# Optimization experiments

Hardware: AMD Instinct MI355X
Metric: run time of the kernel (lower is better)

## Reference

```python
import jax, jax.numpy as jnp
import numpy as np

B, N, I, H, NT = 512, 21, 256, 1024, 5  # batch, nodes, input, hidden, node types
EPS = 1e-12


def setup_inputs() -> dict:
    key = jax.random.key(0)
    ks = jax.random.split(key, 8)
    stdv = 1.0 / np.sqrt(H)
    return {
        "input": jax.random.normal(ks[0], (B, N, I), jnp.float32),
        "hx": 0.1 * jax.random.normal(ks[1], (B, N, H), jnp.float32),
        "cx": 0.1 * jax.random.normal(ks[2], (B, N, H), jnp.float32),
        "G": jnp.eye(N, dtype=jnp.float32) + 0.01 * jax.random.normal(ks[3], (N, N), jnp.float32),
        "weight_ih": jax.random.uniform(ks[4], (NT, 4 * H, I), jnp.float32, -stdv, stdv),
        "weight_hh": jax.random.uniform(ks[5], (NT, 4 * H, H), jnp.float32, -stdv, stdv),
        "bias_hh": jax.random.uniform(ks[6], (NT, 4 * H), jnp.float32, -stdv, stdv),
        "node_types": jax.random.randint(ks[7], (N,), 0, NT),
        "t": 3,
    }


def _l1_normalize_rows(g):
    # torch.nn.functional.normalize(g, p=1, dim=1)
    return g / jnp.maximum(jnp.sum(jnp.abs(g), axis=1, keepdims=True), EPS)


def _clockwork_phase(hidden_size, dtype):
    p = jnp.arange(hidden_size, dtype=dtype)
    p = p / p[-1] * 8.0 + 1.0
    return jnp.floor(p)  # values in {1..9}


def reference(input, hx, cx, G, weight_ih, weight_hh, bias_hh, node_types, t):
    # learn_influence=True -> gx = L1-row-normalized G
    gx = _l1_normalize_rows(G)

    # per-node-type weight gather: [N, 4H, I], [N, 4H, H], [N, 4H]
    w_ih = weight_ih[node_types]
    w_hh = weight_hh[node_types]
    b_hh = bias_hh[node_types]

    # gmm: einsum('ndo,bnd->bno', w.transpose(-2,-1), x) == einsum('noi,bni->bno', w, x)
    gates = (jnp.einsum('noi,bni->bno', w_ih, input)
             + jnp.einsum('noh,bnh->bno', w_hh, hx)
             + b_hh)
    # graph influence: matmul(gx, gates) over node dim -> [B, N, 4H]
    gates = jnp.einsum('mn,bno->bmo', gx, gates)

    ingate, forgetgate, cellgate, outgate = jnp.split(gates, 4, axis=2)
    ingate = jax.nn.sigmoid(ingate)
    forgetgate = jax.nn.sigmoid(forgetgate)
    cellgate = jnp.tanh(cellgate)
    outgate = jax.nn.sigmoid(outgate)

    phase = _clockwork_phase(hx.shape[-1], cx.dtype)
    c_mask = (jnp.remainder(jnp.float32(t) + 1.0, phase) < 0.01).astype(cx.dtype)

    cy = c_mask * (forgetgate * cx + ingate * cellgate) + (1.0 - c_mask) * cx
    hy = outgate * jnp.tanh(cy)

    # gx = gx + G_add (=0), then re-normalized because learn_influence=True
    gx_out = _l1_normalize_rows(gx)
    return hy, cy, gx_out
```

## Files before the change

kernel.cpp:

```cpp
#include <hip/hip_runtime.h>
#include <hip/hip_bf16.h>
#include <stdint.h>


typedef __bf16 bf16_t;
typedef __bf16 bf16x8 __attribute__((ext_vector_type(8)));
typedef float f32x4 __attribute__((ext_vector_type(4)));

#define NB 512
#define NN 21
#define NI 256
#define NH 1024
#define KDIM 1280
#define ODIM 4096
#define BNH (512ull * 21 * 1024)

__device__ inline void gld16(const void* g, const void* l) {
  __builtin_amdgcn_global_load_lds(
      (const __attribute__((address_space(1))) unsigned int*)g,
      (__attribute__((address_space(3))) unsigned int*)l, 16, 0, 0);
}

__device__ inline float sigmoid_fast(float x) {
  return 1.0f / (1.0f + __expf(-x));
}
__device__ inline float tanh_fast(float x) {
  float ax = fabsf(x);
  float e = __expf(2.0f * ax);
  float t = 1.0f - 2.0f / (e + 1.0f);
  return copysignf(t, x);
}

__global__ void gx_kernel(const float* __restrict__ G, float* __restrict__ gxw,
                          float* __restrict__ gxout) {
  int m = threadIdx.x;
  if (m < NN) {
    float s = 0.f;
    for (int j = 0; j < NN; j++) s += fabsf(G[m * NN + j]);
    s = fmaxf(s, 1e-12f);
    float row[NN];
    float s2 = 0.f;
    for (int j = 0; j < NN; j++) {
      row[j] = G[m * NN + j] / s;
      s2 += fabsf(row[j]);
    }
    s2 = fmaxf(s2, 1e-12f);
    for (int j = 0; j < NN; j++) {
      gxw[m * NN + j] = row[j];
      gxout[m * NN + j] = row[j] / s2;
    }
  }
}

__global__ __launch_bounds__(256) void pack_w(const float* __restrict__ wih,
                                              const float* __restrict__ whh,
                                              bf16_t* __restrict__ Wc) {
  int c = blockIdx.x * 256 + threadIdx.x;
  int k8 = c % (KDIM / 8);
  int row = c / (KDIM / 8);
  int k = k8 * 8;
  const float* src = (k < NI) ? (wih + (size_t)row * NI + k)
                              : (whh + (size_t)row * NH + (k - NI));
  float4 a = *(const float4*)src;
  float4 b = *(const float4*)(src + 4);
  bf16x8 o;
  o[0] = (bf16_t)a.x; o[1] = (bf16_t)a.y; o[2] = (bf16_t)a.z; o[3] = (bf16_t)a.w;
  o[4] = (bf16_t)b.x; o[5] = (bf16_t)b.y; o[6] = (bf16_t)b.z; o[7] = (bf16_t)b.w;
  *(bf16x8*)&Wc[(size_t)c * 8] = o;
}

__global__ __launch_bounds__(256) void pack_x(const float* __restrict__ input,
                                              const float* __restrict__ hx,
                                              bf16_t* __restrict__ Xc) {
  int c = blockIdx.x * 256 + threadIdx.x;
  int k8 = c % (KDIM / 8);
  int rest = c / (KDIM / 8);
  int n = rest / NB;
  int b = rest % NB;
  int k = k8 * 8;
  const float* src = (k < NI) ? (input + ((size_t)b * NN + n) * NI + k)
                              : (hx + ((size_t)b * NN + n) * NH + (k - NI));
  float4 a = *(const float4*)src;
  float4 d = *(const float4*)(src + 4);
  bf16x8 o;
  o[0] = (bf16_t)a.x; o[1] = (bf16_t)a.y; o[2] = (bf16_t)a.z; o[3] = (bf16_t)a.w;
  o[4] = (bf16_t)d.x; o[5] = (bf16_t)d.y; o[6] = (bf16_t)d.z; o[7] = (bf16_t)d.w;
  *(bf16x8*)&Xc[(size_t)c * 8] = o;
}

__global__ __launch_bounds__(256) void gemm_bt(const bf16_t* __restrict__ Xc,
                                               const bf16_t* __restrict__ Wc,
                                               const float* __restrict__ bhh,
                                               const int* __restrict__ node_types,
                                               bf16_t* __restrict__ gates) {
  __shared__ bf16_t As[128 * 32];
  __shared__ bf16_t Bs[128 * 32];

  const int n = blockIdx.z;
  const int tau = node_types[n];
  const bf16_t* A = Xc + (size_t)n * NB * KDIM;
  const bf16_t* B = Wc + (size_t)tau * ODIM * KDIM;

  const int tid = threadIdx.x;
  const int m0 = blockIdx.y * 128;
  const int n0 = blockIdx.x * 128;

  const int lane = tid & 63;
  const int wv = tid >> 6;
  const int wm = (wv >> 1) * 64;
  const int wn = (wv & 1) * 64;
  const int r = lane & 15;
  const int quad = lane >> 4;

  f32x4 acc[4][4];
#pragma unroll
  for (int i = 0; i < 4; i++)
#pragma unroll
    for (int j = 0; j < 4; j++) acc[i][j] = {0.f, 0.f, 0.f, 0.f};

  const int srow = tid >> 2;
  const int schunk = (tid & 3) * 8;

  for (int k0 = 0; k0 < KDIM; k0 += 32) {
    gld16(A + (size_t)(m0 + srow) * KDIM + k0 + schunk, (char*)As + tid * 16);
    gld16(A + (size_t)(m0 + 64 + srow) * KDIM + k0 + schunk, (char*)As + 4096 + tid * 16);
    gld16(B + (size_t)(n0 + srow) * KDIM + k0 + schunk, (char*)Bs + tid * 16);
    gld16(B + (size_t)(n0 + 64 + srow) * KDIM + k0 + schunk, (char*)Bs + 4096 + tid * 16);
    __syncthreads();

    bf16x8 af[4], bfr[4];
#pragma unroll
    for (int i = 0; i < 4; i++)
      af[i] = *(const bf16x8*)&As[(wm + i * 16 + r) * 32 + quad * 8];
#pragma unroll
    for (int j = 0; j < 4; j++)
      bfr[j] = *(const bf16x8*)&Bs[(wn + j * 16 + r) * 32 + quad * 8];
#pragma unroll
    for (int i = 0; i < 4; i++)
#pragma unroll
      for (int j = 0; j < 4; j++)
        acc[i][j] = __builtin_amdgcn_mfma_f32_16x16x32_bf16(af[i], bfr[j], acc[i][j], 0, 0, 0);
    __syncthreads();
  }

  float bv[4];
#pragma unroll
  for (int j = 0; j < 4; j++) bv[j] = bhh[tau * ODIM + n0 + wn + j * 16 + r];
#pragma unroll
  for (int i = 0; i < 4; i++) {
    int brow = m0 + wm + i * 16 + quad * 4;
#pragma unroll
    for (int j = 0; j < 4; j++) {
      int o = n0 + wn + j * 16 + r;
#pragma unroll
      for (int reg = 0; reg < 4; reg++) {
        int b = brow + reg;
        gates[((size_t)b * NN + n) * ODIM + o] = (bf16_t)(acc[i][j][reg] + bv[j]);
      }
    }
  }
}

__global__ __launch_bounds__(256) void mix_lin(bf16_t* __restrict__ gates,
                                               const float* __restrict__ gx) {
  __shared__ float gxs[NN * NN];
  __shared__ bf16_t gs[NN * 512];
  const int tid = threadIdx.x;
  for (int i = tid; i < NN * NN; i += 256) gxs[i] = gx[i];
  const int b = blockIdx.y;
  const int o0 = blockIdx.x * 512;
  const size_t base = (size_t)b * NN * ODIM + o0;

  for (int i = tid; i < NN * 64; i += 256) {
    int n = i / 64, c = i % 64;
    *(bf16x8*)&gs[n * 512 + c * 8] = *(const bf16x8*)&gates[base + (size_t)n * ODIM + c * 8];
  }
  __syncthreads();

  for (int i = tid; i < NN * 64; i += 256) {
    int m = i / 64, c = i % 64;
    float acc[8];
#pragma unroll
    for (int j = 0; j < 8; j++) acc[j] = 0.f;
    for (int n = 0; n < NN; n++) {
      float w = gxs[m * NN + n];
      bf16x8 v = *(const bf16x8*)&gs[n * 512 + c * 8];
#pragma unroll
      for (int j = 0; j < 8; j++) acc[j] += w * (float)v[j];
    }
    bf16x8 o;
#pragma unroll
    for (int j = 0; j < 8; j++) o[j] = (bf16_t)acc[j];
    *(bf16x8*)&gates[base + (size_t)m * ODIM + c * 8] = o;
  }
}

__global__ __launch_bounds__(256) void lstm_pw(const bf16_t* __restrict__ gates,
                                               const float* __restrict__ cx,
                                               const int* __restrict__ t_ptr,
                                               float* __restrict__ out) {
  int idx = blockIdx.x * 256 + threadIdx.x;
  int h8 = idx % 128;
  int bm = idx / 128;
  int h = h8 * 8;
  int t = t_ptr[0];
  size_t gbase = (size_t)bm * ODIM;
  bf16x8 vi = *(const bf16x8*)&gates[gbase + 0 * NH + h];
  bf16x8 vf = *(const bf16x8*)&gates[gbase + 1 * NH + h];
  bf16x8 vc = *(const bf16x8*)&gates[gbase + 2 * NH + h];
  bf16x8 vo = *(const bf16x8*)&gates[gbase + 3 * NH + h];
  size_t off = (size_t)bm * NH + h;
  float4 c0 = *(const float4*)&cx[off];
  float4 c1 = *(const float4*)&cx[off + 4];
  float cxv[8] = {c0.x, c0.y, c0.z, c0.w, c1.x, c1.y, c1.z, c1.w};
  float hy[8], cy[8];
  float tf = (float)(t + 1);
#pragma unroll
  for (int j = 0; j < 8; j++) {
    float phase = floorf(((float)(h + j)) / 1023.0f * 8.0f + 1.0f);
    bool cmask = fmodf(tf, phase) < 0.01f;
    float ig = sigmoid_fast((float)vi[j]);
    float fg = sigmoid_fast((float)vf[j]);
    float cg = tanh_fast((float)vc[j]);
    float og = sigmoid_fast((float)vo[j]);
    float c = cmask ? (fg * cxv[j] + ig * cg) : cxv[j];
    cy[j] = c;
    hy[j] = og * tanh_fast(c);
  }
  *(float4*)&out[off] = make_float4(hy[0], hy[1], hy[2], hy[3]);
  *(float4*)&out[off + 4] = make_float4(hy[4], hy[5], hy[6], hy[7]);
  *(float4*)&out[BNH + off] = make_float4(cy[0], cy[1], cy[2], cy[3]);
  *(float4*)&out[BNH + off + 4] = make_float4(cy[4], cy[5], cy[6], cy[7]);
}

extern "C" void kernel_launch(void* const* d_in, const int* in_sizes, int n_in,
                              void* d_out, int out_size, void* d_ws, size_t ws_size,
                              hipStream_t stream) {
  const float* input = (const float*)d_in[0];
  const float* hx = (const float*)d_in[1];
  const float* cx = (const float*)d_in[2];
  const float* G = (const float*)d_in[3];
  const float* wih = (const float*)d_in[4];
  const float* whh = (const float*)d_in[5];
  const float* bhh = (const float*)d_in[6];
  const int* node_types = (const int*)d_in[7];
  const int* t = (const int*)d_in[8];
  float* out = (float*)d_out;

  char* ws = (char*)d_ws;
  bf16_t* Wc = (bf16_t*)ws;
  bf16_t* Xc = (bf16_t*)(ws + 52428800);
  bf16_t* gates = (bf16_t*)(ws + 79953920);
  float* gxw = (float*)(ws + 168034304);

  gx_kernel<<<1, 64, 0, stream>>>(G, gxw, out + 2 * BNH);
  pack_w<<<(5 * ODIM * KDIM / 8) / 256, 256, 0, stream>>>(wih, whh, Wc);
  pack_x<<<(NN * NB * KDIM / 8) / 256, 256, 0, stream>>>(input, hx, Xc);
  dim3 gg(ODIM / 128, NB / 128, NN);
  gemm_bt<<<gg, 256, 0, stream>>>(Xc, Wc, bhh, node_types, gates);
  dim3 gm(ODIM / 512, NB);
  mix_lin<<<gm, 256, 0, stream>>>(gates, gxw);
  lstm_pw<<<(NB * NN * (NH / 8)) / 256, 256, 0, stream>>>(gates, cx, t, out);
}
```

Before: 457.1 us.

## Merge pack kernels, pipeline larger GEMM tiles, fuse graph mix with LSTM

Three packing kernels become one launch. The GEMM moves to 256x256 tiles with 512 threads, a 4-stage LDS ring buffer with swizzled layout, explicit waitcnt/barrier scheduling and setprio around MFMA bursts. The graph-mixing step and the LSTM pointwise step are fused into one kernel, which removes a bf16 round trip of gates through global memory. The manual pipelining brings synchronisation complexity and high register pressure from 32 accumulators per thread.

```diff
diff --git a/kernel.cpp b/kernel.cpp
--- a/kernel.cpp
+++ b/kernel.cpp
@@ -31,123 +31,170 @@
   return copysignf(t, x);
 }
 
-__global__ void gx_kernel(const float* __restrict__ G, float* __restrict__ gxw,
-                          float* __restrict__ gxout) {
-  int m = threadIdx.x;
-  if (m < NN) {
-    float s = 0.f;
-    for (int j = 0; j < NN; j++) s += fabsf(G[m * NN + j]);
-    s = fmaxf(s, 1e-12f);
-    float row[NN];
-    float s2 = 0.f;
-    for (int j = 0; j < NN; j++) {
-      row[j] = G[m * NN + j] / s;
-      s2 += fabsf(row[j]);
+__device__ inline void wg_barrier() {
+  asm volatile("" ::: "memory");
+  __builtin_amdgcn_s_barrier();
+  asm volatile("" ::: "memory");
+}
+
+__global__ __launch_bounds__(256) void pack_all(
+    const float* __restrict__ wih, const float* __restrict__ whh,
+    const float* __restrict__ input, const float* __restrict__ hx,
+    const float* __restrict__ G, bf16_t* __restrict__ Wc,
+    bf16_t* __restrict__ Xc, float* __restrict__ gxw,
+    float* __restrict__ gxout) {
+  const int bx = blockIdx.x;
+  const int tid = threadIdx.x;
+  if (bx < 12800) {
+    int c = bx * 256 + tid;
+    int k8 = c % (KDIM / 8);
+    int row = c / (KDIM / 8);
+    int k = k8 * 8;
+    const float* src = (k < NI) ? (wih + (size_t)row * NI + k)
+                                : (whh + (size_t)row * NH + (k - NI));
+    float4 a = *(const float4*)src;
+    float4 b = *(const float4*)(src + 4);
+    bf16x8 o;
+    o[0] = (bf16_t)a.x; o[1] = (bf16_t)a.y; o[2] = (bf16_t)a.z; o[3] = (bf16_t)a.w;
+    o[4] = (bf16_t)b.x; o[5] = (bf16_t)b.y; o[6] = (bf16_t)b.z; o[7] = (bf16_t)b.w;
+    *(bf16x8*)&Wc[(size_t)c * 8] = o;
+  } else if (bx < 19520) {
+    int c = (bx - 12800) * 256 + tid;
+    int k8 = c % (KDIM / 8);
+    int rest = c / (KDIM / 8);
+    int n = rest / NB;
+    int b = rest % NB;
+    int k = k8 * 8;
+    const float* src = (k < NI) ? (input + ((size_t)b * NN + n) * NI + k)
+                                : (hx + ((size_t)b * NN + n) * NH + (k - NI));
+    float4 a = *(const float4*)src;
+    float4 d = *(const float4*)(src + 4);
+    bf16x8 o;
+    o[0] = (bf16_t)a.x; o[1] = (bf16_t)a.y; o[2] = (bf16_t)a.z; o[3] = (bf16_t)a.w;
+    o[4] = (bf16_t)d.x; o[5] = (bf16_t)d.y; o[6] = (bf16_t)d.z; o[7] = (bf16_t)d.w;
+    *(bf16x8*)&Xc[(size_t)c * 8] = o;
+  } else {
+    int m = tid;
+    if (m < NN) {
+      float s = 0.f;
+      for (int j = 0; j < NN; j++) s += fabsf(G[m * NN + j]);
+      s = fmaxf(s, 1e-12f);
+      float row[NN];
+      float s2 = 0.f;
+      for (int j = 0; j < NN; j++) {
+        row[j] = G[m * NN + j] / s;
+        s2 += fabsf(row[j]);
+      }
+      s2 = fmaxf(s2, 1e-12f);
+      for (int j = 0; j < NN; j++) {
+        gxw[m * NN + j] = row[j];
+        gxout[m * NN + j] = row[j] / s2;
+      }
     }
-    s2 = fmaxf(s2, 1e-12f);
-    for (int j = 0; j < NN; j++) {
-      gxw[m * NN + j] = row[j];
-      gxout[m * NN + j] = row[j] / s2;
-    }
-  }
-}
-
-__global__ __launch_bounds__(256) void pack_w(const float* __restrict__ wih,
-                                              const float* __restrict__ whh,
-                                              bf16_t* __restrict__ Wc) {
-  int c = blockIdx.x * 256 + threadIdx.x;
-  int k8 = c % (KDIM / 8);
-  int row = c / (KDIM / 8);
-  int k = k8 * 8;
-  const float* src = (k < NI) ? (wih + (size_t)row * NI + k)
-                              : (whh + (size_t)row * NH + (k - NI));
-  float4 a = *(const float4*)src;
-  float4 b = *(const float4*)(src + 4);
-  bf16x8 o;
-  o[0] = (bf16_t)a.x; o[1] = (bf16_t)a.y; o[2] = (bf16_t)a.z; o[3] = (bf16_t)a.w;
-  o[4] = (bf16_t)b.x; o[5] = (bf16_t)b.y; o[6] = (bf16_t)b.z; o[7] = (bf16_t)b.w;
-  *(bf16x8*)&Wc[(size_t)c * 8] = o;
-}
-
-__global__ __launch_bounds__(256) void pack_x(const float* __restrict__ input,
-                                              const float* __restrict__ hx,
-                                              bf16_t* __restrict__ Xc) {
-  int c = blockIdx.x * 256 + threadIdx.x;
-  int k8 = c % (KDIM / 8);
-  int rest = c / (KDIM / 8);
-  int n = rest / NB;
-  int b = rest % NB;
-  int k = k8 * 8;
-  const float* src = (k < NI) ? (input + ((size_t)b * NN + n) * NI + k)
-                              : (hx + ((size_t)b * NN + n) * NH + (k - NI));
-  float4 a = *(const float4*)src;
-  float4 d = *(const float4*)(src + 4);
-  bf16x8 o;
-  o[0] = (bf16_t)a.x; o[1] = (bf16_t)a.y; o[2] = (bf16_t)a.z; o[3] = (bf16_t)a.w;
-  o[4] = (bf16_t)d.x; o[5] = (bf16_t)d.y; o[6] = (bf16_t)d.z; o[7] = (bf16_t)d.w;
-  *(bf16x8*)&Xc[(size_t)c * 8] = o;
-}
-
-__global__ __launch_bounds__(256) void gemm_bt(const bf16_t* __restrict__ Xc,
-                                               const bf16_t* __restrict__ Wc,
-                                               const float* __restrict__ bhh,
-                                               const int* __restrict__ node_types,
-                                               bf16_t* __restrict__ gates) {
-  __shared__ bf16_t As[128 * 32];
-  __shared__ bf16_t Bs[128 * 32];
+  }
+}
+
+__global__ __launch_bounds__(512, 2) void gemm_bt(
+    const bf16_t* __restrict__ Xc, const bf16_t* __restrict__ Wc,
+    const float* __restrict__ bhh, const int* __restrict__ node_types,
+    bf16_t* __restrict__ gates) {
+  __shared__ char lds[4 * 32768];
 
   const int n = blockIdx.z;
   const int tau = node_types[n];
   const bf16_t* A = Xc + (size_t)n * NB * KDIM;
-  const bf16_t* B = Wc + (size_t)tau * ODIM * KDIM;
+  const bf16_t* Bw = Wc + (size_t)tau * ODIM * KDIM;
 
   const int tid = threadIdx.x;
-  const int m0 = blockIdx.y * 128;
-  const int n0 = blockIdx.x * 128;
-
   const int lane = tid & 63;
-  const int wv = tid >> 6;
-  const int wm = (wv >> 1) * 64;
-  const int wn = (wv & 1) * 64;
+  const int w = tid >> 6;
+  const int wm = (w & 1) * 128;
+  const int wn = (w >> 1) * 64;
   const int r = lane & 15;
   const int quad = lane >> 4;
 
-  f32x4 acc[4][4];
-#pragma unroll
-  for (int i = 0; i < 4; i++)
+  const int m0 = blockIdx.y * 256;
+  const int n0 = blockIdx.x * 256;
+
+  const int ga = ((wm + r) >> 1) & 3;
+  const int gb = ((wn + r) >> 1) & 3;
+  const int aoff = (wm + r) * 64 + ((quad ^ ga) * 16);
+  const int boff = 16384 + (wn + r) * 64 + ((quad ^ gb) * 16);
+
+  const int ca = w * 128 + lane;
+  const int cb = ca + 64;
+  const int rA0 = ca >> 2, cA0 = (ca & 3) ^ ((rA0 >> 1) & 3);
+  const int rA1 = cb >> 2, cA1 = (cb & 3) ^ ((rA1 >> 1) & 3);
+  const bf16_t* gA0 = A + (size_t)(m0 + rA0) * KDIM + cA0 * 8;
+  const bf16_t* gA1 = A + (size_t)(m0 + rA1) * KDIM + cA1 * 8;
+  const bf16_t* gB0 = Bw + (size_t)(n0 + rA0) * KDIM + cA0 * 8;
+  const bf16_t* gB1 = Bw + (size_t)(n0 + rA1) * KDIM + cA1 * 8;
+  const int dA0 = ca * 16, dA1 = cb * 16;
+
+  f32x4 acc[8][4];
+#pragma unroll
+  for (int i = 0; i < 8; i++)
 #pragma unroll
     for (int j = 0; j < 4; j++) acc[i][j] = {0.f, 0.f, 0.f, 0.f};
 
-  const int srow = tid >> 2;
-  const int schunk = (tid & 3) * 8;
-
-  for (int k0 = 0; k0 < KDIM; k0 += 32) {
-    gld16(A + (size_t)(m0 + srow) * KDIM + k0 + schunk, (char*)As + tid * 16);
-    gld16(A + (size_t)(m0 + 64 + srow) * KDIM + k0 + schunk, (char*)As + 4096 + tid * 16);
-    gld16(B + (size_t)(n0 + srow) * KDIM + k0 + schunk, (char*)Bs + tid * 16);
-    gld16(B + (size_t)(n0 + 64 + srow) * KDIM + k0 + schunk, (char*)Bs + 4096 + tid * 16);
-    __syncthreads();
-
-    bf16x8 af[4], bfr[4];
+  {
+    char* L0 = lds;
+    char* L1 = lds + 32768;
+    gld16(gA0, L0 + dA0);          gld16(gA1, L0 + dA1);
+    gld16(gB0, L0 + 16384 + dA0);  gld16(gB1, L0 + 16384 + dA1);
+    gld16(gA0 + 32, L1 + dA0);         gld16(gA1 + 32, L1 + dA1);
+    gld16(gB0 + 32, L1 + 16384 + dA0); gld16(gB1 + 32, L1 + 16384 + dA1);
+    asm volatile("s_waitcnt vmcnt(4)" ::: "memory");
+    wg_barrier();
+  }
+
+  for (int t = 0; t < 40; ++t) {
+    const char* P = lds + (t & 3) * 32768;
+    char* Wd = lds + ((t + 2) & 3) * 32768;
+    const bool st = (t < 38);
+    const int kk = (t + 2) * 32;
+    bf16x8 a0[4], a1[4], b0[4];
+
+#pragma unroll
+    for (int i = 0; i < 4; i++) a0[i] = *(const bf16x8*)(P + aoff + i * 1024);
+#pragma unroll
+    for (int j = 0; j < 4; j++) b0[j] = *(const bf16x8*)(P + boff + j * 1024);
+    if (st) { gld16(gA0 + kk, Wd + dA0); gld16(gA1 + kk, Wd + dA1); }
+    wg_barrier();
+    asm volatile("s_waitcnt lgkmcnt(0)" ::: "memory");
+    __builtin_amdgcn_sched_barrier(0);
+    __builtin_amdgcn_s_setprio(1);
 #pragma unroll
     for (int i = 0; i < 4; i++)
-      af[i] = *(const bf16x8*)&As[(wm + i * 16 + r) * 32 + quad * 8];
-#pragma unroll
-    for (int j = 0; j < 4; j++)
-      bfr[j] = *(const bf16x8*)&Bs[(wn + j * 16 + r) * 32 + quad * 8];
+#pragma unroll
+      for (int j = 0; j < 4; j++)
+        acc[i][j] = __builtin_amdgcn_mfma_f32_16x16x32_bf16(a0[i], b0[j], acc[i][j], 0, 0, 0);
+    __builtin_amdgcn_s_setprio(0);
+    wg_barrier();
+
+#pragma unroll
+    for (int i = 0; i < 4; i++) a1[i] = *(const bf16x8*)(P + aoff + 4096 + i * 1024);
+    if (st) { gld16(gB0 + kk, Wd + 16384 + dA0); gld16(gB1 + kk, Wd + 16384 + dA1); }
+    wg_barrier();
+    asm volatile("s_waitcnt lgkmcnt(0)" ::: "memory");
+    __builtin_amdgcn_sched_barrier(0);
+    __builtin_amdgcn_s_setprio(1);
 #pragma unroll
     for (int i = 0; i < 4; i++)
 #pragma unroll
       for (int j = 0; j < 4; j++)
-        acc[i][j] = __builtin_amdgcn_mfma_f32_16x16x32_bf16(af[i], bfr[j], acc[i][j], 0, 0, 0);
-    __syncthreads();
+        acc[4 + i][j] = __builtin_amdgcn_mfma_f32_16x16x32_bf16(a1[i], b0[j], acc[4 + i][j], 0, 0, 0);
+    __builtin_amdgcn_s_setprio(0);
+    if (t < 38)       asm volatile("s_waitcnt vmcnt(4)" ::: "memory");
+    else if (t == 38) asm volatile("s_waitcnt vmcnt(0)" ::: "memory");
+    wg_barrier();
   }
 
   float bv[4];
 #pragma unroll
   for (int j = 0; j < 4; j++) bv[j] = bhh[tau * ODIM + n0 + wn + j * 16 + r];
 #pragma unroll
-  for (int i = 0; i < 4; i++) {
+  for (int i = 0; i < 8; i++) {
     int brow = m0 + wm + i * 16 + quad * 4;
 #pragma unroll
     for (int j = 0; j < 4; j++) {
@@ -161,76 +208,73 @@
   }
 }
 
-__global__ __launch_bounds__(256) void mix_lin(bf16_t* __restrict__ gates,
-                                               const float* __restrict__ gx) {
-  __shared__ float gxs[NN * NN];
-  __shared__ bf16_t gs[NN * 512];
+template <int M0C, int CH>
+__device__ inline void mix_chunk(const bf16_t (*gs)[4][256],
+                                 const float* __restrict__ gx,
+                                 const float* __restrict__ cx,
+                                 float* __restrict__ out, int b, int h, int tid,
+                                 bool cmask) {
+  float a[CH][4];
+#pragma unroll
+  for (int mm = 0; mm < CH; mm++) {
+    a[mm][0] = 0.f; a[mm][1] = 0.f; a[mm][2] = 0.f; a[mm][3] = 0.f;
+  }
+  for (int nn = 0; nn < NN; nn++) {
+    float v0 = (float)gs[nn][0][tid];
+    float v1 = (float)gs[nn][1][tid];
+    float v2 = (float)gs[nn][2][tid];
+    float v3 = (float)gs[nn][3][tid];
+#pragma unroll
+    for (int mm = 0; mm < CH; mm++) {
+      float wgt = gx[(M0C + mm) * NN + nn];
+      a[mm][0] = fmaf(wgt, v0, a[mm][0]);
+      a[mm][1] = fmaf(wgt, v1, a[mm][1]);
+      a[mm][2] = fmaf(wgt, v2, a[mm][2]);
+      a[mm][3] = fmaf(wgt, v3, a[mm][3]);
+    }
+  }
+#pragma unroll
+  for (int mm = 0; mm < CH; mm++) {
+    int m = M0C + mm;
+    size_t off = ((size_t)b * NN + m) * NH + h;
+    float c0 = cx[off];
+    float ig = sigmoid_fast(a[mm][0]);
+    float fg = sigmoid_fast(a[mm][1]);
+    float cg = tanh_fast(a[mm][2]);
+    float og = sigmoid_fast(a[mm][3]);
+    float c = cmask ? fmaf(fg, c0, ig * cg) : c0;
+    out[off] = og * tanh_fast(c);
+    out[BNH + off] = c;
+  }
+}
+
+__global__ __launch_bounds__(256) void mix_lstm(const bf16_t* __restrict__ gates,
+                                                const float* __restrict__ gx,
+                                                const float* __restrict__ cx,
+                                                const int* __restrict__ t_ptr,
+                                                float* __restrict__ out) {
+  __shared__ bf16_t gs[NN][4][256];
   const int tid = threadIdx.x;
-  for (int i = tid; i < NN * NN; i += 256) gxs[i] = gx[i];
   const int b = blockIdx.y;
-  const int o0 = blockIdx.x * 512;
-  const size_t base = (size_t)b * NN * ODIM + o0;
-
-  for (int i = tid; i < NN * 64; i += 256) {
-    int n = i / 64, c = i % 64;
-    *(bf16x8*)&gs[n * 512 + c * 8] = *(const bf16x8*)&gates[base + (size_t)n * ODIM + c * 8];
+  const int h0 = blockIdx.x * 256;
+  const size_t gb = (size_t)b * NN * ODIM;
+  for (int i = tid; i < NN * 4 * 32; i += 256) {
+    int nn = i >> 7;
+    int rem = i & 127;
+    int g = rem >> 5;
+    int c = rem & 31;
+    *(bf16x8*)&gs[nn][g][c * 8] =
+        *(const bf16x8*)&gates[gb + (size_t)nn * ODIM + g * NH + h0 + c * 8];
   }
   __syncthreads();
 
-  for (int i = tid; i < NN * 64; i += 256) {
-    int m = i / 64, c = i % 64;
-    float acc[8];
-#pragma unroll
-    for (int j = 0; j < 8; j++) acc[j] = 0.f;
-    for (int n = 0; n < NN; n++) {
-      float w = gxs[m * NN + n];
-      bf16x8 v = *(const bf16x8*)&gs[n * 512 + c * 8];
-#pragma unroll
-      for (int j = 0; j < 8; j++) acc[j] += w * (float)v[j];
-    }
-    bf16x8 o;
-#pragma unroll
-    for (int j = 0; j < 8; j++) o[j] = (bf16_t)acc[j];
-    *(bf16x8*)&gates[base + (size_t)m * ODIM + c * 8] = o;
-  }
-}
-
-__global__ __launch_bounds__(256) void lstm_pw(const bf16_t* __restrict__ gates,
-                                               const float* __restrict__ cx,
-                                               const int* __restrict__ t_ptr,
-                                               float* __restrict__ out) {
-  int idx = blockIdx.x * 256 + threadIdx.x;
-  int h8 = idx % 128;
-  int bm = idx / 128;
-  int h = h8 * 8;
-  int t = t_ptr[0];
-  size_t gbase = (size_t)bm * ODIM;
-  bf16x8 vi = *(const bf16x8*)&gates[gbase + 0 * NH + h];
-  bf16x8 vf = *(const bf16x8*)&gates[gbase + 1 * NH + h];
-  bf16x8 vc = *(const bf16x8*)&gates[gbase + 2 * NH + h];
-  bf16x8 vo = *(const bf16x8*)&gates[gbase + 3 * NH + h];
-  size_t off = (size_t)bm * NH + h;
-  float4 c0 = *(const float4*)&cx[off];
-  float4 c1 = *(const float4*)&cx[off + 4];
-  float cxv[8] = {c0.x, c0.y, c0.z, c0.w, c1.x, c1.y, c1.z, c1.w};
-  float hy[8], cy[8];
-  float tf = (float)(t + 1);
-#pragma unroll
-  for (int j = 0; j < 8; j++) {
-    float phase = floorf(((float)(h + j)) / 1023.0f * 8.0f + 1.0f);
-    bool cmask = fmodf(tf, phase) < 0.01f;
-    float ig = sigmoid_fast((float)vi[j]);
-    float fg = sigmoid_fast((float)vf[j]);
-    float cg = tanh_fast((float)vc[j]);
-    float og = sigmoid_fast((float)vo[j]);
-    float c = cmask ? (fg * cxv[j] + ig * cg) : cxv[j];
-    cy[j] = c;
-    hy[j] = og * tanh_fast(c);
-  }
-  *(float4*)&out[off] = make_float4(hy[0], hy[1], hy[2], hy[3]);
-  *(float4*)&out[off + 4] = make_float4(hy[4], hy[5], hy[6], hy[7]);
-  *(float4*)&out[BNH + off] = make_float4(cy[0], cy[1], cy[2], cy[3]);
-  *(float4*)&out[BNH + off + 4] = make_float4(cy[4], cy[5], cy[6], cy[7]);
+  const int h = h0 + tid;
+  const float tf = (float)(t_ptr[0] + 1);
+  float phase = floorf((float)h / 1023.0f * 8.0f + 1.0f);
+  bool cmask = fmodf(tf, phase) < 0.01f;
+
+  mix_chunk<0, 11>(gs, gx, cx, out, b, h, tid, cmask);
+  mix_chunk<11, 10>(gs, gx, cx, out, b, h, tid, cmask);
 }
 
 extern "C" void kernel_launch(void* const* d_in, const int* in_sizes, int n_in,
@@ -253,12 +297,10 @@
   bf16_t* gates = (bf16_t*)(ws + 79953920);
   float* gxw = (float*)(ws + 168034304);
 
-  gx_kernel<<<1, 64, 0, stream>>>(G, gxw, out + 2 * BNH);
-  pack_w<<<(5 * ODIM * KDIM / 8) / 256, 256, 0, stream>>>(wih, whh, Wc);
-  pack_x<<<(NN * NB * KDIM / 8) / 256, 256, 0, stream>>>(input, hx, Xc);
-  dim3 gg(ODIM / 128, NB / 128, NN);
-  gemm_bt<<<gg, 256, 0, stream>>>(Xc, Wc, bhh, node_types, gates);
-  dim3 gm(ODIM / 512, NB);
-  mix_lin<<<gm, 256, 0, stream>>>(gates, gxw);
-  lstm_pw<<<(NB * NN * (NH / 8)) / 256, 256, 0, stream>>>(gates, cx, t, out);
-}
+  pack_all<<<19521, 256, 0, stream>>>(wih, whh, input, hx, G, Wc, Xc, gxw,
+                                      out + 2 * BNH);
+  dim3 gg(ODIM / 256, NB / 256, NN);
+  gemm_bt<<<gg, 512, 0, stream>>>(Xc, Wc, bhh, node_types, gates);
+  dim3 gm(NH / 256, NB);
+  mix_lstm<<<gm, 256, 0, stream>>>(gates, gxw, cx, t, out);
+}
```

Result: faster. 426.8 us (-6.6%).
